# Kernel tuning notes

Measured on AMD Instinct MI355X. Metric: run time of the kernel, lower is better.

Reference implementation:

```python
import jax, jax.numpy as jnp
import numpy as np

HEADS = 16

def setup_inputs() -> dict:
    key = jax.random.key(0)
    k1, k2, k3, k4 = jax.random.split(key, 4)
    B, T, S, W = 2, 2048, 2048, 1024
    x = jax.random.normal(k1, (B, T, W), dtype=jnp.float32)
    cond_k = jax.random.normal(k2, (B, S, W), dtype=jnp.float32)
    cond_v = jax.random.normal(k3, (B, S, W), dtype=jnp.float32)
    w_proj = jax.random.normal(k4, (W, W), dtype=jnp.float32) * 0.02
    b_proj = jnp.zeros((W,), dtype=jnp.float32)
    return {"x": x, "cond_k": cond_k, "cond_v": cond_v, "w_proj": w_proj, "b_proj": b_proj}

def reference(x, cond_k, cond_v, w_proj, b_proj):
    B, T, W = x.shape
    S = cond_k.shape[1]
    H = HEADS
    d = W // H
    scale = 1.0 / jnp.sqrt(jnp.sqrt(jnp.float32(d)))  # applied to both q and k
    q = x.reshape(B, T, H, d) * scale
    k = cond_k.reshape(B, S, H, d) * scale
    v = cond_v.reshape(B, S, H, d)
    # scores: [B, H, T, S]
    scores = jnp.einsum('bthd,bshd->bhts', q, k)
    w = jax.nn.softmax(scores.astype(jnp.float32), axis=-1).astype(scores.dtype)
    out = jnp.einsum('bhts,bshd->bthd', w, v).reshape(B, T, W)
    # c_proj: torch Linear -> x @ W.T + b
    return out @ w_proj.T + b_proj
```

## Files before the change

kernel.cpp:

```cpp
#include <hip/hip_runtime.h>

#define Bn 2
#define Hn 16
#define Tn 2048
#define Sn 2048
#define Wd 1024
#define Dh 64

typedef __attribute__((ext_vector_type(8))) short s16x8;
typedef __attribute__((ext_vector_type(4))) short s16x4;
typedef __attribute__((ext_vector_type(4))) float f32x4;
typedef __attribute__((ext_vector_type(4))) unsigned u32x4;

#define MFMA(a, b, c) __builtin_amdgcn_mfma_f32_16x16x32_bf16((a), (b), (c), 0, 0, 0)

__device__ __forceinline__ s16x8 ld8(const short* p) { return *(const s16x8*)p; }

__device__ __forceinline__ short f2bf(float f) {
    unsigned u = __builtin_bit_cast(unsigned, f);
    u += 0x7FFFu + ((u >> 16) & 1u);
    return (short)(u >> 16);
}

__device__ __forceinline__ unsigned cvtpk(float lo, float hi) {
    unsigned r;
    asm("v_cvt_pk_bf16_f32 %0, %1, %2" : "=v"(r) : "v"(lo), "v"(hi));
    return r;
}

__device__ __forceinline__ void gl_lds(const short* g, short* lds) {
    __builtin_amdgcn_global_load_lds(
        (const __attribute__((address_space(1))) void*)g,
        (__attribute__((address_space(3))) void*)lds, 16, 0, 0);
}

__global__ __launch_bounds__(256) void prep(const float* __restrict__ ck,
                                            const float* __restrict__ cv,
                                            const float* __restrict__ wp,
                                            short* __restrict__ kp,
                                            short* __restrict__ vp,
                                            short* __restrict__ wb)
{
    __shared__ short T[64][72];
    const int blk = blockIdx.x;
    const int tid = threadIdx.x;
    if (blk < 2048) {
        const int isV = blk >> 10;
        const int c   = blk & 1023;
        const int bh = c >> 5, sc = c & 31;
        const int b = bh >> 4, h = bh & 15;
        const float* src = (isV ? cv : ck) + (size_t)(b * Sn + sc * 64) * Wd + h * Dh;
#pragma unroll
        for (int i = 0; i < 4; ++i) {
            int f = i * 256 + tid, sr = f >> 4, c4 = f & 15;
            float4 v = *(const float4*)(src + (size_t)sr * Wd + c4 * 4);
            s16x4 o;
            o[0] = f2bf(v.x); o[1] = f2bf(v.y); o[2] = f2bf(v.z); o[3] = f2bf(v.w);
            *(s16x4*)&T[sr][c4 * 4] = o;
        }
        __syncthreads();
        const int rt = tid >> 6;
        const int l = tid & 63, quad = l >> 4, l16 = l & 15;
        if (!isV) {
            size_t base = ((size_t)((bh * 128 + sc * 4 + rt) * 2)) * 512 + l * 8;
            *(s16x8*)(kp + base)       = *(const s16x8*)&T[rt * 16 + l16][quad * 8];
            *(s16x8*)(kp + base + 512) = *(const s16x8*)&T[rt * 16 + l16][32 + quad * 8];
        } else {
#pragma unroll
            for (int g = 0; g < 2; ++g) {
                s16x8 o;
#pragma unroll
                for (int j = 0; j < 8; ++j) {
                    int s = 32 * g + 16 * (j >> 2) + quad * 4 + (j & 3);
                    o[j] = T[s][rt * 16 + l16];
                }
                *(s16x8*)(vp + ((size_t)((bh * 32 + sc) * 8 + rt * 2 + g)) * 512 + l * 8) = o;
            }
        }
    } else {
        int i = ((blk - 2048) * 256 + tid) * 8;
        float4 a = *(const float4*)(wp + i);
        float4 b = *(const float4*)(wp + i + 4);
        s16x8 o;
        o[0] = f2bf(a.x); o[1] = f2bf(a.y); o[2] = f2bf(a.z); o[3] = f2bf(a.w);
        o[4] = f2bf(b.x); o[5] = f2bf(b.y); o[6] = f2bf(b.z); o[7] = f2bf(b.w);
        *(s16x8*)(wb + i) = o;
    }
}

__global__ __launch_bounds__(512, 4) void attn_fused(
    const float* __restrict__ x, const short* __restrict__ kp,
    const short* __restrict__ vt, short* __restrict__ ao)
{
    __shared__ alignas(16) short Ks[2][2][8 * 512];
    __shared__ alignas(16) short Vs[2][2][8 * 512];

    const int tid  = threadIdx.x;
    const int w    = tid >> 6;
    const int l    = tid & 63;
    const int quad = l >> 4;
    const int l16  = l & 15;
    const int wq   = w & 3;
    const int pr   = w >> 2;

    const int bh = blockIdx.x & 31;
    const int qt = blockIdx.x >> 5;
    const int b  = bh >> 4, h = bh & 15;

    const int qrow0 = qt * 128 + wq * 32;

    const short* kp_h = kp + (size_t)bh * 131072;
    const short* vp_h = vt + (size_t)bh * 131072;

    gl_lds(kp_h + ((size_t)(0 * 8 + w)) * 512 + l * 8, &Ks[0][0][w * 512]);
    gl_lds(vp_h + ((size_t)(0 * 8 + w)) * 512 + l * 8, &Vs[0][0][w * 512]);
    gl_lds(kp_h + ((size_t)(1 * 8 + w)) * 512 + l * 8, &Ks[0][1][w * 512]);
    gl_lds(vp_h + ((size_t)(1 * 8 + w)) * 512 + l * 8, &Vs[0][1][w * 512]);

    const float SQ = 0.125f * 1.4426950408889634f;
    s16x8 aq[2][2];
#pragma unroll
    for (int mi = 0; mi < 2; ++mi)
#pragma unroll
        for (int c = 0; c < 2; ++c) {
            const float* p = x + (size_t)(b * Tn + qrow0 + mi * 16 + l16) * Wd
                               + h * Dh + c * 32 + quad * 8;
            float4 a = ((const float4*)p)[0], bb = ((const float4*)p)[1];
            s16x8 o;
            o[0] = f2bf(a.x * SQ); o[1] = f2bf(a.y * SQ); o[2] = f2bf(a.z * SQ); o[3] = f2bf(a.w * SQ);
            o[4] = f2bf(bb.x * SQ); o[5] = f2bf(bb.y * SQ); o[6] = f2bf(bb.z * SQ); o[7] = f2bf(bb.w * SQ);
            aq[mi][c] = o;
        }

    f32x4 oacc[2][4], dnacc[2];
#pragma unroll
    for (int mi = 0; mi < 2; ++mi) {
#pragma unroll
        for (int nt = 0; nt < 4; ++nt) {
            oacc[mi][nt][0] = 0.f; oacc[mi][nt][1] = 0.f;
            oacc[mi][nt][2] = 0.f; oacc[mi][nt][3] = 0.f;
        }
        dnacc[mi][0] = 0.f; dnacc[mi][1] = 0.f;
        dnacc[mi][2] = 0.f; dnacc[mi][3] = 0.f;
    }

    s16x8 ones;
#pragma unroll
    for (int j = 0; j < 8; ++j) ones[j] = (short)0x3F80;

    const f32x4 z = {0.f, 0.f, 0.f, 0.f};
    const int NSIT = Sn / 128;

    asm volatile("s_waitcnt vmcnt(0)" ::: "memory");
    __syncthreads();

    for (int t = 0; t < NSIT; ++t) {
        const int sb = t & 1;

        if (t + 1 < NSIT) {
            const size_t c0 = (size_t)(2 * t + 2) * 8;
            gl_lds(kp_h + (c0 + w) * 512 + l * 8,     &Ks[sb ^ 1][0][w * 512]);
            gl_lds(vp_h + (c0 + w) * 512 + l * 8,     &Vs[sb ^ 1][0][w * 512]);
            gl_lds(kp_h + (c0 + 8 + w) * 512 + l * 8, &Ks[sb ^ 1][1][w * 512]);
            gl_lds(vp_h + (c0 + 8 + w) * 512 + l * 8, &Vs[sb ^ 1][1][w * 512]);
        }

        const short* Kb = &Ks[sb][pr][0];
        const short* Vb = &Vs[sb][pr][0];

        s16x8 kf[4][2];
#pragma unroll
        for (int sj = 0; sj < 4; ++sj)
#pragma unroll
            for (int g = 0; g < 2; ++g)
                kf[sj][g] = *(const s16x8*)&Kb[(sj * 2 + g) * 512 + l * 8];

        f32x4 sc[2][4];
        __builtin_amdgcn_s_setprio(1);
#pragma unroll
        for (int sj = 0; sj < 4; ++sj)
#pragma unroll
            for (int mi = 0; mi < 2; ++mi) {
                sc[mi][sj] = MFMA(kf[sj][0], aq[mi][0], z);
                sc[mi][sj] = MFMA(kf[sj][1], aq[mi][1], sc[mi][sj]);
            }
        __builtin_amdgcn_s_setprio(0);

        s16x8 ap[2][2];
#pragma unroll
        for (int mi = 0; mi < 2; ++mi) {
            float ex[4][4];
#pragma unroll
            for (int sj = 0; sj < 4; ++sj)
#pragma unroll
                for (int r = 0; r < 4; ++r)
                    ex[sj][r] = __builtin_amdgcn_exp2f(sc[mi][sj][r]);
#pragma unroll
            for (int g = 0; g < 2; ++g) {
                u32x4 pk;
                pk[0] = cvtpk(ex[2 * g][0],     ex[2 * g][1]);
                pk[1] = cvtpk(ex[2 * g][2],     ex[2 * g][3]);
                pk[2] = cvtpk(ex[2 * g + 1][0], ex[2 * g + 1][1]);
                pk[3] = cvtpk(ex[2 * g + 1][2], ex[2 * g + 1][3]);
                ap[mi][g] = __builtin_bit_cast(s16x8, pk);
            }
        }

        s16x8 vf[4][2];
#pragma unroll
        for (int nt = 0; nt < 4; ++nt)
#pragma unroll
            for (int g = 0; g < 2; ++g)
                vf[nt][g] = *(const s16x8*)&Vb[(nt * 2 + g) * 512 + l * 8];

        __builtin_amdgcn_s_setprio(1);
#pragma unroll
        for (int mi = 0; mi < 2; ++mi) {
            dnacc[mi] = MFMA(ap[mi][0], ones, dnacc[mi]);
            dnacc[mi] = MFMA(ap[mi][1], ones, dnacc[mi]);
        }
#pragma unroll
        for (int mi = 0; mi < 2; ++mi)
#pragma unroll
            for (int nt = 0; nt < 4; ++nt) {
                oacc[mi][nt] = MFMA(ap[mi][0], vf[nt][0], oacc[mi][nt]);
                oacc[mi][nt] = MFMA(ap[mi][1], vf[nt][1], oacc[mi][nt]);
            }
        __builtin_amdgcn_s_setprio(0);

        asm volatile("s_waitcnt vmcnt(0)" ::: "memory");
        __syncthreads();
    }

    float* ob = (float*)&Ks[0][0][0];
    float* db = (float*)&Vs[0][0][0];
    if (pr == 1) {
#pragma unroll
        for (int mi = 0; mi < 2; ++mi) {
#pragma unroll
            for (int r = 0; r < 4; ++r) {
                int ql = wq * 32 + mi * 16 + quad * 4 + r;
#pragma unroll
                for (int nt = 0; nt < 4; ++nt)
                    ob[ql * 64 + nt * 16 + l16] = oacc[mi][nt][r];
                if (l16 == 0) db[ql] = dnacc[mi][r];
            }
        }
    }
    __syncthreads();
    if (pr == 0) {
#pragma unroll
        for (int mi = 0; mi < 2; ++mi)
#pragma unroll
            for (int r = 0; r < 4; ++r) {
                int ql = wq * 32 + mi * 16 + quad * 4 + r;
                float inv = 1.0f / (dnacc[mi][r] + db[ql]);
                int t = qrow0 + mi * 16 + quad * 4 + r;
#pragma unroll
                for (int nt = 0; nt < 4; ++nt) {
                    float v = oacc[mi][nt][r] + ob[ql * 64 + nt * 16 + l16];
                    ao[(size_t)(b * Tn + t) * Wd + h * Dh + nt * 16 + l16] = f2bf(v * inv);
                }
            }
    }
}

#define LSTR2 72

__global__ __launch_bounds__(512, 4) void proj_gemm(
    const short* __restrict__ A, const short* __restrict__ Wb,
    const float* __restrict__ bias, float* __restrict__ out)
{
    __shared__ alignas(16) short As[2][128 * LSTR2];
    __shared__ alignas(16) short Bs[2][64 * LSTR2];

    const int tid  = threadIdx.x;
    const int w    = tid >> 6;
    const int l    = tid & 63;
    const int quad = l >> 4;
    const int l16  = l & 15;

    const int bn = blockIdx.x & 15;
    const int bm = blockIdx.x >> 4;
    const int m0 = bm * 128;
    const int n0 = bn * 64;
    const int wm = (w & 3) * 32;
    const int wn = (w >> 2) * 32;

    const int rr = tid >> 3;
    const int sg = tid & 7;

    f32x4 acc[2][2];
#pragma unroll
    for (int mi = 0; mi < 2; ++mi)
#pragma unroll
        for (int nt = 0; nt < 2; ++nt) {
            acc[mi][nt][0] = 0.f; acc[mi][nt][1] = 0.f;
            acc[mi][nt][2] = 0.f; acc[mi][nt][3] = 0.f;
        }

    s16x8 ra0 = ld8(A  + (size_t)(m0 + rr) * Wd + sg * 8);
    s16x8 ra1 = ld8(A  + (size_t)(m0 + 64 + rr) * Wd + sg * 8);
    s16x8 rb  = ld8(Wb + (size_t)(n0 + rr) * Wd + sg * 8);
    *(s16x8*)&As[0][rr * LSTR2 + sg * 8]        = ra0;
    *(s16x8*)&As[0][(rr + 64) * LSTR2 + sg * 8] = ra1;
    *(s16x8*)&Bs[0][rr * LSTR2 + sg * 8]        = rb;
    __syncthreads();

    for (int k0 = 0; k0 < Wd; k0 += 64) {
        const int p = (k0 >> 6) & 1;

        if (k0 + 64 < Wd) {
            ra0 = ld8(A  + (size_t)(m0 + rr) * Wd + k0 + 64 + sg * 8);
            ra1 = ld8(A  + (size_t)(m0 + 64 + rr) * Wd + k0 + 64 + sg * 8);
            rb  = ld8(Wb + (size_t)(n0 + rr) * Wd + k0 + 64 + sg * 8);
        }

        s16x8 a[2][2], bw[2][2];
#pragma unroll
        for (int mi = 0; mi < 2; ++mi)
#pragma unroll
            for (int ks = 0; ks < 2; ++ks)
                a[mi][ks] = *(const s16x8*)&As[p][(wm + mi * 16 + l16) * LSTR2 + ks * 32 + quad * 8];
#pragma unroll
        for (int nt = 0; nt < 2; ++nt)
#pragma unroll
            for (int ks = 0; ks < 2; ++ks)
                bw[nt][ks] = *(const s16x8*)&Bs[p][(wn + nt * 16 + l16) * LSTR2 + ks * 32 + quad * 8];

        __builtin_amdgcn_s_setprio(1);
#pragma unroll
        for (int mi = 0; mi < 2; ++mi)
#pragma unroll
            for (int nt = 0; nt < 2; ++nt) {
                acc[mi][nt] = MFMA(a[mi][0], bw[nt][0], acc[mi][nt]);
                acc[mi][nt] = MFMA(a[mi][1], bw[nt][1], acc[mi][nt]);
            }
        __builtin_amdgcn_s_setprio(0);

        if (k0 + 64 < Wd) {
            *(s16x8*)&As[p ^ 1][rr * LSTR2 + sg * 8]        = ra0;
            *(s16x8*)&As[p ^ 1][(rr + 64) * LSTR2 + sg * 8] = ra1;
            *(s16x8*)&Bs[p ^ 1][rr * LSTR2 + sg * 8]        = rb;
        }
        __syncthreads();
    }

#pragma unroll
    for (int nt = 0; nt < 2; ++nt) {
        float bv = bias[n0 + wn + nt * 16 + l16];
#pragma unroll
        for (int mi = 0; mi < 2; ++mi)
#pragma unroll
            for (int r = 0; r < 4; ++r)
                out[(size_t)(m0 + wm + mi * 16 + quad * 4 + r) * Wd + n0 + wn + nt * 16 + l16] =
                    acc[mi][nt][r] + bv;
    }
}

extern "C" void kernel_launch(void* const* d_in, const int* in_sizes, int n_in,
                              void* d_out, int out_size, void* d_ws, size_t ws_size,
                              hipStream_t stream) {
    const float* x  = (const float*)d_in[0];
    const float* ck = (const float*)d_in[1];
    const float* cv = (const float*)d_in[2];
    const float* wp = (const float*)d_in[3];
    const float* bp = (const float*)d_in[4];

    const int nX = Bn * Tn * Wd;
    const int nW = Wd * Wd;

    short* kpb = (short*)d_ws;
    short* vpb = kpb + nX;
    short* wbb = vpb + nX;
    short* am  = wbb + nW;

    prep<<<dim3(2048 + nW / 2048), dim3(256), 0, stream>>>(ck, cv, wp, kpb, vpb, wbb);

    attn_fused<<<dim3(Bn * Hn * (Tn / 128)), dim3(512), 0, stream>>>(x, kpb, vpb, am);
    proj_gemm<<<dim3((Bn * Tn / 128) * (Wd / 64)), dim3(512), 0, stream>>>(
        am, wbb, bp, (float*)d_out);
}
```

Measured before the change: 148.9 us.

## Pre-pack projection weights into MFMA fragments and stream A via global_load_lds

The prep kernel now converts w_proj into per-16-row MFMA fragment tiles, so proj_gemm can load B operands directly from global memory into registers with no LDS staging. The A operand is brought in with direct global-to-LDS loads into an XOR-swizzled unpadded layout instead of going through registers. This removes the B shared-memory buffer and the register round trip for A. The cost is a full vmcnt wait each iteration and B fragments read from global/L2 by every block that needs them.

```diff
diff --git a/kernel.cpp b/kernel.cpp
--- a/kernel.cpp
+++ b/kernel.cpp
@@ -41,7 +41,7 @@
                                             short* __restrict__ vp,
                                             short* __restrict__ wb)
 {
-    __shared__ short T[64][72];
+    __shared__ short T[64 * 72];
     const int blk = blockIdx.x;
     const int tid = threadIdx.x;
     if (blk < 2048) {
@@ -56,15 +56,15 @@
             float4 v = *(const float4*)(src + (size_t)sr * Wd + c4 * 4);
             s16x4 o;
             o[0] = f2bf(v.x); o[1] = f2bf(v.y); o[2] = f2bf(v.z); o[3] = f2bf(v.w);
-            *(s16x4*)&T[sr][c4 * 4] = o;
+            *(s16x4*)&T[sr * 72 + c4 * 4] = o;
         }
         __syncthreads();
         const int rt = tid >> 6;
         const int l = tid & 63, quad = l >> 4, l16 = l & 15;
         if (!isV) {
             size_t base = ((size_t)((bh * 128 + sc * 4 + rt) * 2)) * 512 + l * 8;
-            *(s16x8*)(kp + base)       = *(const s16x8*)&T[rt * 16 + l16][quad * 8];
-            *(s16x8*)(kp + base + 512) = *(const s16x8*)&T[rt * 16 + l16][32 + quad * 8];
+            *(s16x8*)(kp + base)       = *(const s16x8*)&T[(rt * 16 + l16) * 72 + quad * 8];
+            *(s16x8*)(kp + base + 512) = *(const s16x8*)&T[(rt * 16 + l16) * 72 + 32 + quad * 8];
         } else {
 #pragma unroll
             for (int g = 0; g < 2; ++g) {
@@ -72,19 +72,30 @@
 #pragma unroll
                 for (int j = 0; j < 8; ++j) {
                     int s = 32 * g + 16 * (j >> 2) + quad * 4 + (j & 3);
-                    o[j] = T[s][rt * 16 + l16];
+                    o[j] = T[s * 72 + rt * 16 + l16];
                 }
                 *(s16x8*)(vp + ((size_t)((bh * 32 + sc) * 8 + rt * 2 + g)) * 512 + l * 8) = o;
             }
         }
     } else {
-        int i = ((blk - 2048) * 256 + tid) * 8;
-        float4 a = *(const float4*)(wp + i);
-        float4 b = *(const float4*)(wp + i + 4);
-        s16x8 o;
-        o[0] = f2bf(a.x); o[1] = f2bf(a.y); o[2] = f2bf(a.z); o[3] = f2bf(a.w);
-        o[4] = f2bf(b.x); o[5] = f2bf(b.y); o[6] = f2bf(b.z); o[7] = f2bf(b.w);
-        *(s16x8*)(wb + i) = o;
+        const int c = blk - 2048;
+        const int tr = c >> 4, tc = c & 15;
+#pragma unroll
+        for (int i = 0; i < 4; ++i) {
+            int f = i * 256 + tid, sr = f >> 4, c4 = f & 15;
+            float4 v = *(const float4*)(wp + (size_t)(tr * 64 + sr) * Wd + tc * 64 + c4 * 4);
+            s16x4 o;
+            o[0] = f2bf(v.x); o[1] = f2bf(v.y); o[2] = f2bf(v.z); o[3] = f2bf(v.w);
+            *(s16x4*)&T[sr * 72 + c4 * 4] = o;
+        }
+        __syncthreads();
+        const int rt = tid >> 6;
+        const int l = tid & 63, quad = l >> 4, l16 = l & 15;
+#pragma unroll
+        for (int gl = 0; gl < 2; ++gl) {
+            size_t base = ((size_t)((tr * 4 + rt) * 32 + tc * 2 + gl)) * 512 + l * 8;
+            *(s16x8*)(wb + base) = *(const s16x8*)&T[(rt * 16 + l16) * 72 + gl * 32 + quad * 8];
+        }
     }
 }
 
@@ -265,14 +276,11 @@
     }
 }
 
-#define LSTR2 72
-
 __global__ __launch_bounds__(512, 4) void proj_gemm(
-    const short* __restrict__ A, const short* __restrict__ Wb,
+    const short* __restrict__ A, const short* __restrict__ wbp,
     const float* __restrict__ bias, float* __restrict__ out)
 {
-    __shared__ alignas(16) short As[2][128 * LSTR2];
-    __shared__ alignas(16) short Bs[2][64 * LSTR2];
+    __shared__ alignas(16) short As[2][128 * 64];
 
     const int tid  = threadIdx.x;
     const int w    = tid >> 6;
@@ -286,9 +294,10 @@
     const int n0 = bn * 64;
     const int wm = (w & 3) * 32;
     const int wn = (w >> 2) * 32;
-
-    const int rr = tid >> 3;
-    const int sg = tid & 7;
+    const int n16b = bn * 4 + (w >> 2) * 2;
+
+    const int rl0 = w * 16 + (l >> 3);
+    const int b16 = l & 7;
 
     f32x4 acc[2][2];
 #pragma unroll
@@ -299,34 +308,43 @@
             acc[mi][nt][2] = 0.f; acc[mi][nt][3] = 0.f;
         }
 
-    s16x8 ra0 = ld8(A  + (size_t)(m0 + rr) * Wd + sg * 8);
-    s16x8 ra1 = ld8(A  + (size_t)(m0 + 64 + rr) * Wd + sg * 8);
-    s16x8 rb  = ld8(Wb + (size_t)(n0 + rr) * Wd + sg * 8);
-    *(s16x8*)&As[0][rr * LSTR2 + sg * 8]        = ra0;
-    *(s16x8*)&As[0][(rr + 64) * LSTR2 + sg * 8] = ra1;
-    *(s16x8*)&Bs[0][rr * LSTR2 + sg * 8]        = rb;
+#pragma unroll
+    for (int u = 0; u < 2; ++u) {
+        int row = rl0 + u * 8;
+        gl_lds(A + (size_t)(m0 + row) * Wd + ((b16 ^ (row & 7)) * 8),
+               &As[0][(w * 16 + u * 8) * 64]);
+    }
+    asm volatile("s_waitcnt vmcnt(0)" ::: "memory");
     __syncthreads();
 
     for (int k0 = 0; k0 < Wd; k0 += 64) {
         const int p = (k0 >> 6) & 1;
+        const int kg = k0 >> 5;
+
+        s16x8 bw[2][2];
+#pragma unroll
+        for (int nt = 0; nt < 2; ++nt)
+#pragma unroll
+            for (int ks = 0; ks < 2; ++ks)
+                bw[nt][ks] = ld8(wbp + ((size_t)(n16b + nt) * 32 + kg + ks) * 512 + l * 8);
 
         if (k0 + 64 < Wd) {
-            ra0 = ld8(A  + (size_t)(m0 + rr) * Wd + k0 + 64 + sg * 8);
-            ra1 = ld8(A  + (size_t)(m0 + 64 + rr) * Wd + k0 + 64 + sg * 8);
-            rb  = ld8(Wb + (size_t)(n0 + rr) * Wd + k0 + 64 + sg * 8);
-        }
-
-        s16x8 a[2][2], bw[2][2];
-#pragma unroll
-        for (int mi = 0; mi < 2; ++mi)
+#pragma unroll
+            for (int u = 0; u < 2; ++u) {
+                int row = rl0 + u * 8;
+                gl_lds(A + (size_t)(m0 + row) * Wd + k0 + 64 + ((b16 ^ (row & 7)) * 8),
+                       &As[p ^ 1][(w * 16 + u * 8) * 64]);
+            }
+        }
+
+        s16x8 a[2][2];
+#pragma unroll
+        for (int mi = 0; mi < 2; ++mi) {
+            const int row = wm + mi * 16 + l16;
 #pragma unroll
             for (int ks = 0; ks < 2; ++ks)
-                a[mi][ks] = *(const s16x8*)&As[p][(wm + mi * 16 + l16) * LSTR2 + ks * 32 + quad * 8];
-#pragma unroll
-        for (int nt = 0; nt < 2; ++nt)
-#pragma unroll
-            for (int ks = 0; ks < 2; ++ks)
-                bw[nt][ks] = *(const s16x8*)&Bs[p][(wn + nt * 16 + l16) * LSTR2 + ks * 32 + quad * 8];
+                a[mi][ks] = *(const s16x8*)&As[p][row * 64 + ((ks * 4 + quad) ^ (row & 7)) * 8];
+        }
 
         __builtin_amdgcn_s_setprio(1);
 #pragma unroll
@@ -338,11 +356,7 @@
             }
         __builtin_amdgcn_s_setprio(0);
 
-        if (k0 + 64 < Wd) {
-            *(s16x8*)&As[p ^ 1][rr * LSTR2 + sg * 8]        = ra0;
-            *(s16x8*)&As[p ^ 1][(rr + 64) * LSTR2 + sg * 8] = ra1;
-            *(s16x8*)&Bs[p ^ 1][rr * LSTR2 + sg * 8]        = rb;
-        }
+        asm volatile("s_waitcnt vmcnt(0)" ::: "memory");
         __syncthreads();
     }
 
@@ -375,7 +389,7 @@
     short* wbb = vpb + nX;
     short* am  = wbb + nW;
 
-    prep<<<dim3(2048 + nW / 2048), dim3(256), 0, stream>>>(ck, cv, wp, kpb, vpb, wbb);
+    prep<<<dim3(2048 + 256), dim3(256), 0, stream>>>(ck, cv, wp, kpb, vpb, wbb);
 
     attn_fused<<<dim3(Bn * Hn * (Tn / 128)), dim3(512), 0, stream>>>(x, kpb, vpb, am);
     proj_gemm<<<dim3((Bn * Tn / 128) * (Wd / 64)), dim3(512), 0, stream>>>(
```

New measurement: 150.2 us. No clear change (+0.9%).

## Fuse prep, attention and projection into one persistent kernel with grid barriers

Applied to the files above, without the earlier changes.

Merges the three kernels into a single persistent kernel of 512 blocks that runs the bf16 conversion/relayout work in a strided task loop, crosses a software global barrier, runs attention, crosses another barrier, and then runs the output projection GEMM. The shared memory is unified into one buffer reused by each phase. This removes two kernel launch boundaries and their tail/drain gaps, but adds atomic spin barriers and requires all 512 blocks to be co-resident (occupancy 4 blocks per CU assumed), and the prep phase now uses only half the threads for the store step.

```diff
diff --git a/kernel.cpp b/kernel.cpp
--- a/kernel.cpp
+++ b/kernel.cpp
@@ -6,6 +6,7 @@
 #define Sn 2048
 #define Wd 1024
 #define Dh 64
+#define NBLK 512
 
 typedef __attribute__((ext_vector_type(8))) short s16x8;
 typedef __attribute__((ext_vector_type(4))) short s16x4;
@@ -34,327 +35,352 @@
         (__attribute__((address_space(3))) void*)lds, 16, 0, 0);
 }
 
-__global__ __launch_bounds__(256) void prep(const float* __restrict__ ck,
-                                            const float* __restrict__ cv,
-                                            const float* __restrict__ wp,
-                                            short* __restrict__ kp,
-                                            short* __restrict__ vp,
-                                            short* __restrict__ wb)
+__global__ void binit(unsigned* bar) { bar[0] = 0u; bar[1] = 0u; }
+
+__device__ __forceinline__ void gbar(unsigned* bar) {
+    __syncthreads();
+    if (threadIdx.x == 0) {
+        __builtin_amdgcn_fence(__ATOMIC_RELEASE, "agent");
+        unsigned g = __hip_atomic_load(&bar[1], __ATOMIC_ACQUIRE,
+                                       __HIP_MEMORY_SCOPE_AGENT);
+        unsigned arr = __hip_atomic_fetch_add(&bar[0], 1u, __ATOMIC_ACQ_REL,
+                                              __HIP_MEMORY_SCOPE_AGENT);
+        if (arr == NBLK - 1u) {
+            __hip_atomic_store(&bar[0], 0u, __ATOMIC_RELAXED,
+                               __HIP_MEMORY_SCOPE_AGENT);
+            __hip_atomic_fetch_add(&bar[1], 1u, __ATOMIC_RELEASE,
+                                   __HIP_MEMORY_SCOPE_AGENT);
+        } else {
+            long spins = 0;
+            while (__hip_atomic_load(&bar[1], __ATOMIC_ACQUIRE,
+                                     __HIP_MEMORY_SCOPE_AGENT) == g) {
+                __builtin_amdgcn_s_sleep(2);
+                if (++spins > (1L << 26)) break;
+            }
+        }
+    }
+    __syncthreads();
+    __builtin_amdgcn_fence(__ATOMIC_ACQUIRE, "agent");
+}
+
+__global__ __launch_bounds__(512, 4) void fused(
+    const float* __restrict__ x,  const float* __restrict__ ck,
+    const float* __restrict__ cv, const float* __restrict__ wp,
+    const float* __restrict__ bias,
+    short* __restrict__ kp, short* __restrict__ vp, short* __restrict__ wb,
+    short* __restrict__ am, float* __restrict__ out, unsigned* __restrict__ bar)
 {
-    __shared__ short T[64][72];
-    const int blk = blockIdx.x;
-    const int tid = threadIdx.x;
-    if (blk < 2048) {
-        const int isV = blk >> 10;
-        const int c   = blk & 1023;
-        const int bh = c >> 5, sc = c & 31;
-        const int b = bh >> 4, h = bh & 15;
-        const float* src = (isV ? cv : ck) + (size_t)(b * Sn + sc * 64) * Wd + h * Dh;
-#pragma unroll
-        for (int i = 0; i < 4; ++i) {
-            int f = i * 256 + tid, sr = f >> 4, c4 = f & 15;
-            float4 v = *(const float4*)(src + (size_t)sr * Wd + c4 * 4);
-            s16x4 o;
-            o[0] = f2bf(v.x); o[1] = f2bf(v.y); o[2] = f2bf(v.z); o[3] = f2bf(v.w);
-            *(s16x4*)&T[sr][c4 * 4] = o;
-        }
-        __syncthreads();
-        const int rt = tid >> 6;
-        const int l = tid & 63, quad = l >> 4, l16 = l & 15;
-        if (!isV) {
-            size_t base = ((size_t)((bh * 128 + sc * 4 + rt) * 2)) * 512 + l * 8;
-            *(s16x8*)(kp + base)       = *(const s16x8*)&T[rt * 16 + l16][quad * 8];
-            *(s16x8*)(kp + base + 512) = *(const s16x8*)&T[rt * 16 + l16][32 + quad * 8];
-        } else {
-#pragma unroll
-            for (int g = 0; g < 2; ++g) {
-                s16x8 o;
-#pragma unroll
-                for (int j = 0; j < 8; ++j) {
-                    int s = 32 * g + 16 * (j >> 2) + quad * 4 + (j & 3);
-                    o[j] = T[s][rt * 16 + l16];
-                }
-                *(s16x8*)(vp + ((size_t)((bh * 32 + sc) * 8 + rt * 2 + g)) * 512 + l * 8) = o;
-            }
-        }
-    } else {
-        int i = ((blk - 2048) * 256 + tid) * 8;
-        float4 a = *(const float4*)(wp + i);
-        float4 b = *(const float4*)(wp + i + 4);
-        s16x8 o;
-        o[0] = f2bf(a.x); o[1] = f2bf(a.y); o[2] = f2bf(a.z); o[3] = f2bf(a.w);
-        o[4] = f2bf(b.x); o[5] = f2bf(b.y); o[6] = f2bf(b.z); o[7] = f2bf(b.w);
-        *(s16x8*)(wb + i) = o;
-    }
-}
-
-__global__ __launch_bounds__(512, 4) void attn_fused(
-    const float* __restrict__ x, const short* __restrict__ kp,
-    const short* __restrict__ vt, short* __restrict__ ao)
-{
-    __shared__ alignas(16) short Ks[2][2][8 * 512];
-    __shared__ alignas(16) short Vs[2][2][8 * 512];
+    __shared__ alignas(16) short U[32768];
 
     const int tid  = threadIdx.x;
+    const int bid  = blockIdx.x;
     const int w    = tid >> 6;
     const int l    = tid & 63;
     const int quad = l >> 4;
     const int l16  = l & 15;
-    const int wq   = w & 3;
-    const int pr   = w >> 2;
-
-    const int bh = blockIdx.x & 31;
-    const int qt = blockIdx.x >> 5;
-    const int b  = bh >> 4, h = bh & 15;
-
-    const int qrow0 = qt * 128 + wq * 32;
-
-    const short* kp_h = kp + (size_t)bh * 131072;
-    const short* vp_h = vt + (size_t)bh * 131072;
-
-    gl_lds(kp_h + ((size_t)(0 * 8 + w)) * 512 + l * 8, &Ks[0][0][w * 512]);
-    gl_lds(vp_h + ((size_t)(0 * 8 + w)) * 512 + l * 8, &Vs[0][0][w * 512]);
-    gl_lds(kp_h + ((size_t)(1 * 8 + w)) * 512 + l * 8, &Ks[0][1][w * 512]);
-    gl_lds(vp_h + ((size_t)(1 * 8 + w)) * 512 + l * 8, &Vs[0][1][w * 512]);
-
-    const float SQ = 0.125f * 1.4426950408889634f;
-    s16x8 aq[2][2];
-#pragma unroll
-    for (int mi = 0; mi < 2; ++mi)
-#pragma unroll
-        for (int c = 0; c < 2; ++c) {
-            const float* p = x + (size_t)(b * Tn + qrow0 + mi * 16 + l16) * Wd
-                               + h * Dh + c * 32 + quad * 8;
-            float4 a = ((const float4*)p)[0], bb = ((const float4*)p)[1];
+
+    for (int task = bid; task < 2304; task += 512) {
+        __syncthreads();
+        if (task < 2048) {
+            const int isV = task >> 10;
+            const int c   = task & 1023;
+            const int bh = c >> 5, sc = c & 31;
+            const int b = bh >> 4, h = bh & 15;
+            const float* src = (isV ? cv : ck) + (size_t)(b * Sn + sc * 64) * Wd + h * Dh;
+#pragma unroll
+            for (int i = 0; i < 2; ++i) {
+                int f = i * 512 + tid, sr = f >> 4, c4 = f & 15;
+                float4 v = *(const float4*)(src + (size_t)sr * Wd + c4 * 4);
+                s16x4 o;
+                o[0] = f2bf(v.x); o[1] = f2bf(v.y); o[2] = f2bf(v.z); o[3] = f2bf(v.w);
+                *(s16x4*)&U[sr * 72 + c4 * 4] = o;
+            }
+            __syncthreads();
+            if (tid < 256) {
+                const int rt = tid >> 6;
+                if (!isV) {
+                    size_t base = ((size_t)((bh * 128 + sc * 4 + rt) * 2)) * 512 + l * 8;
+                    *(s16x8*)(kp + base)       = *(const s16x8*)&U[(rt * 16 + l16) * 72 + quad * 8];
+                    *(s16x8*)(kp + base + 512) = *(const s16x8*)&U[(rt * 16 + l16) * 72 + 32 + quad * 8];
+                } else {
+#pragma unroll
+                    for (int g = 0; g < 2; ++g) {
+                        s16x8 o;
+#pragma unroll
+                        for (int j = 0; j < 8; ++j) {
+                            int s = 32 * g + 16 * (j >> 2) + quad * 4 + (j & 3);
+                            o[j] = U[s * 72 + rt * 16 + l16];
+                        }
+                        *(s16x8*)(vp + ((size_t)((bh * 32 + sc) * 8 + rt * 2 + g)) * 512 + l * 8) = o;
+                    }
+                }
+            }
+        } else {
+            int i = ((task - 2048) * 512 + tid) * 8;
+            float4 a = *(const float4*)(wp + i);
+            float4 b2 = *(const float4*)(wp + i + 4);
             s16x8 o;
-            o[0] = f2bf(a.x * SQ); o[1] = f2bf(a.y * SQ); o[2] = f2bf(a.z * SQ); o[3] = f2bf(a.w * SQ);
-            o[4] = f2bf(bb.x * SQ); o[5] = f2bf(bb.y * SQ); o[6] = f2bf(bb.z * SQ); o[7] = f2bf(bb.w * SQ);
-            aq[mi][c] = o;
-        }
-
-    f32x4 oacc[2][4], dnacc[2];
-#pragma unroll
-    for (int mi = 0; mi < 2; ++mi) {
-#pragma unroll
-        for (int nt = 0; nt < 4; ++nt) {
-            oacc[mi][nt][0] = 0.f; oacc[mi][nt][1] = 0.f;
-            oacc[mi][nt][2] = 0.f; oacc[mi][nt][3] = 0.f;
-        }
-        dnacc[mi][0] = 0.f; dnacc[mi][1] = 0.f;
-        dnacc[mi][2] = 0.f; dnacc[mi][3] = 0.f;
+            o[0] = f2bf(a.x); o[1] = f2bf(a.y); o[2] = f2bf(a.z); o[3] = f2bf(a.w);
+            o[4] = f2bf(b2.x); o[5] = f2bf(b2.y); o[6] = f2bf(b2.z); o[7] = f2bf(b2.w);
+            *(s16x8*)(wb + i) = o;
+        }
     }
-
-    s16x8 ones;
-#pragma unroll
-    for (int j = 0; j < 8; ++j) ones[j] = (short)0x3F80;
-
-    const f32x4 z = {0.f, 0.f, 0.f, 0.f};
-    const int NSIT = Sn / 128;
-
-    asm volatile("s_waitcnt vmcnt(0)" ::: "memory");
-    __syncthreads();
-
-    for (int t = 0; t < NSIT; ++t) {
-        const int sb = t & 1;
-
-        if (t + 1 < NSIT) {
-            const size_t c0 = (size_t)(2 * t + 2) * 8;
-            gl_lds(kp_h + (c0 + w) * 512 + l * 8,     &Ks[sb ^ 1][0][w * 512]);
-            gl_lds(vp_h + (c0 + w) * 512 + l * 8,     &Vs[sb ^ 1][0][w * 512]);
-            gl_lds(kp_h + (c0 + 8 + w) * 512 + l * 8, &Ks[sb ^ 1][1][w * 512]);
-            gl_lds(vp_h + (c0 + 8 + w) * 512 + l * 8, &Vs[sb ^ 1][1][w * 512]);
-        }
-
-        const short* Kb = &Ks[sb][pr][0];
-        const short* Vb = &Vs[sb][pr][0];
-
-        s16x8 kf[4][2];
-#pragma unroll
-        for (int sj = 0; sj < 4; ++sj)
-#pragma unroll
-            for (int g = 0; g < 2; ++g)
-                kf[sj][g] = *(const s16x8*)&Kb[(sj * 2 + g) * 512 + l * 8];
-
-        f32x4 sc[2][4];
-        __builtin_amdgcn_s_setprio(1);
-#pragma unroll
-        for (int sj = 0; sj < 4; ++sj)
-#pragma unroll
-            for (int mi = 0; mi < 2; ++mi) {
-                sc[mi][sj] = MFMA(kf[sj][0], aq[mi][0], z);
-                sc[mi][sj] = MFMA(kf[sj][1], aq[mi][1], sc[mi][sj]);
-            }
-        __builtin_amdgcn_s_setprio(0);
-
-        s16x8 ap[2][2];
+    gbar(bar);
+
+    {
+        short* const KsB = U;
+        short* const VsB = U + 16384;
+
+        const int wq = w & 3;
+        const int pr = w >> 2;
+
+        const int bh = bid & 31;
+        const int qt = bid >> 5;
+        const int b  = bh >> 4, h = bh & 15;
+
+        const int qrow0 = qt * 128 + wq * 32;
+
+        const short* kp_h = kp + (size_t)bh * 131072;
+        const short* vp_h = vp + (size_t)bh * 131072;
+
+        gl_lds(kp_h + ((size_t)(0 * 8 + w)) * 512 + l * 8, KsB + 0 * 4096 + w * 512);
+        gl_lds(vp_h + ((size_t)(0 * 8 + w)) * 512 + l * 8, VsB + 0 * 4096 + w * 512);
+        gl_lds(kp_h + ((size_t)(1 * 8 + w)) * 512 + l * 8, KsB + 1 * 4096 + w * 512);
+        gl_lds(vp_h + ((size_t)(1 * 8 + w)) * 512 + l * 8, VsB + 1 * 4096 + w * 512);
+
+        const float SQ = 0.125f * 1.4426950408889634f;
+        s16x8 aq[2][2];
+#pragma unroll
+        for (int mi = 0; mi < 2; ++mi)
+#pragma unroll
+            for (int c = 0; c < 2; ++c) {
+                const float* p = x + (size_t)(b * Tn + qrow0 + mi * 16 + l16) * Wd
+                                   + h * Dh + c * 32 + quad * 8;
+                float4 a = ((const float4*)p)[0], bb = ((const float4*)p)[1];
+                s16x8 o;
+                o[0] = f2bf(a.x * SQ); o[1] = f2bf(a.y * SQ); o[2] = f2bf(a.z * SQ); o[3] = f2bf(a.w * SQ);
+                o[4] = f2bf(bb.x * SQ); o[5] = f2bf(bb.y * SQ); o[6] = f2bf(bb.z * SQ); o[7] = f2bf(bb.w * SQ);
+                aq[mi][c] = o;
+            }
+
+        f32x4 oacc[2][4], dnacc[2];
 #pragma unroll
         for (int mi = 0; mi < 2; ++mi) {
-            float ex[4][4];
-#pragma unroll
-            for (int sj = 0; sj < 4; ++sj)
-#pragma unroll
-                for (int r = 0; r < 4; ++r)
-                    ex[sj][r] = __builtin_amdgcn_exp2f(sc[mi][sj][r]);
-#pragma unroll
-            for (int g = 0; g < 2; ++g) {
-                u32x4 pk;
-                pk[0] = cvtpk(ex[2 * g][0],     ex[2 * g][1]);
-                pk[1] = cvtpk(ex[2 * g][2],     ex[2 * g][3]);
-                pk[2] = cvtpk(ex[2 * g + 1][0], ex[2 * g + 1][1]);
-                pk[3] = cvtpk(ex[2 * g + 1][2], ex[2 * g + 1][3]);
-                ap[mi][g] = __builtin_bit_cast(s16x8, pk);
-            }
-        }
-
-        s16x8 vf[4][2];
-#pragma unroll
-        for (int nt = 0; nt < 4; ++nt)
-#pragma unroll
-            for (int g = 0; g < 2; ++g)
-                vf[nt][g] = *(const s16x8*)&Vb[(nt * 2 + g) * 512 + l * 8];
-
-        __builtin_amdgcn_s_setprio(1);
-#pragma unroll
-        for (int mi = 0; mi < 2; ++mi) {
-            dnacc[mi] = MFMA(ap[mi][0], ones, dnacc[mi]);
-            dnacc[mi] = MFMA(ap[mi][1], ones, dnacc[mi]);
-        }
-#pragma unroll
-        for (int mi = 0; mi < 2; ++mi)
 #pragma unroll
             for (int nt = 0; nt < 4; ++nt) {
-                oacc[mi][nt] = MFMA(ap[mi][0], vf[nt][0], oacc[mi][nt]);
-                oacc[mi][nt] = MFMA(ap[mi][1], vf[nt][1], oacc[mi][nt]);
-            }
-        __builtin_amdgcn_s_setprio(0);
+                oacc[mi][nt][0] = 0.f; oacc[mi][nt][1] = 0.f;
+                oacc[mi][nt][2] = 0.f; oacc[mi][nt][3] = 0.f;
+            }
+            dnacc[mi][0] = 0.f; dnacc[mi][1] = 0.f;
+            dnacc[mi][2] = 0.f; dnacc[mi][3] = 0.f;
+        }
+
+        s16x8 ones;
+#pragma unroll
+        for (int j = 0; j < 8; ++j) ones[j] = (short)0x3F80;
+
+        const f32x4 z = {0.f, 0.f, 0.f, 0.f};
+        const int NSIT = Sn / 128;
 
         asm volatile("s_waitcnt vmcnt(0)" ::: "memory");
         __syncthreads();
+
+        for (int t = 0; t < NSIT; ++t) {
+            const int sb = t & 1;
+
+            if (t + 1 < NSIT) {
+                const size_t c0 = (size_t)(2 * t + 2) * 8;
+                gl_lds(kp_h + (c0 + w) * 512 + l * 8,     KsB + ((sb ^ 1) * 2 + 0) * 4096 + w * 512);
+                gl_lds(vp_h + (c0 + w) * 512 + l * 8,     VsB + ((sb ^ 1) * 2 + 0) * 4096 + w * 512);
+                gl_lds(kp_h + (c0 + 8 + w) * 512 + l * 8, KsB + ((sb ^ 1) * 2 + 1) * 4096 + w * 512);
+                gl_lds(vp_h + (c0 + 8 + w) * 512 + l * 8, VsB + ((sb ^ 1) * 2 + 1) * 4096 + w * 512);
+            }
+
+            const short* Kb = KsB + (sb * 2 + pr) * 4096;
+            const short* Vb = VsB + (sb * 2 + pr) * 4096;
+
+            s16x8 kf[4][2];
+#pragma unroll
+            for (int sj = 0; sj < 4; ++sj)
+#pragma unroll
+                for (int g = 0; g < 2; ++g)
+                    kf[sj][g] = *(const s16x8*)&Kb[(sj * 2 + g) * 512 + l * 8];
+
+            f32x4 sc[2][4];
+            __builtin_amdgcn_s_setprio(1);
+#pragma unroll
+            for (int sj = 0; sj < 4; ++sj)
+#pragma unroll
+                for (int mi = 0; mi < 2; ++mi) {
+                    sc[mi][sj] = MFMA(kf[sj][0], aq[mi][0], z);
+                    sc[mi][sj] = MFMA(kf[sj][1], aq[mi][1], sc[mi][sj]);
+                }
+            __builtin_amdgcn_s_setprio(0);
+
+            s16x8 ap[2][2];
+#pragma unroll
+            for (int mi = 0; mi < 2; ++mi) {
+                float ex[4][4];
+#pragma unroll
+                for (int sj = 0; sj < 4; ++sj)
+#pragma unroll
+                    for (int r = 0; r < 4; ++r)
+                        ex[sj][r] = __builtin_amdgcn_exp2f(sc[mi][sj][r]);
+#pragma unroll
+                for (int g = 0; g < 2; ++g) {
+                    u32x4 pk;
+                    pk[0] = cvtpk(ex[2 * g][0],     ex[2 * g][1]);
+                    pk[1] = cvtpk(ex[2 * g][2],     ex[2 * g][3]);
+                    pk[2] = cvtpk(ex[2 * g + 1][0], ex[2 * g + 1][1]);
+                    pk[3] = cvtpk(ex[2 * g + 1][2], ex[2 * g + 1][3]);
+                    ap[mi][g] = __builtin_bit_cast(s16x8, pk);
+                }
+            }
+
+            s16x8 vf[4][2];
+#pragma unroll
+            for (int nt = 0; nt < 4; ++nt)
+#pragma unroll
+                for (int g = 0; g < 2; ++g)
+                    vf[nt][g] = *(const s16x8*)&Vb[(nt * 2 + g) * 512 + l * 8];
+
+            __builtin_amdgcn_s_setprio(1);
+#pragma unroll
+            for (int mi = 0; mi < 2; ++mi) {
+                dnacc[mi] = MFMA(ap[mi][0], ones, dnacc[mi]);
+                dnacc[mi] = MFMA(ap[mi][1], ones, dnacc[mi]);
+            }
+#pragma unroll
+            for (int mi = 0; mi < 2; ++mi)
+#pragma unroll
+                for (int nt = 0; nt < 4; ++nt) {
+                    oacc[mi][nt] = MFMA(ap[mi][0], vf[nt][0], oacc[mi][nt]);
+                    oacc[mi][nt] = MFMA(ap[mi][1], vf[nt][1], oacc[mi][nt]);
+                }
+            __builtin_amdgcn_s_setprio(0);
+
+            asm volatile("s_waitcnt vmcnt(0)" ::: "memory");
+            __syncthreads();
+        }
+
+        float* ob = (float*)U;
+        float* db = (float*)(U + 16384);
+        if (pr == 1) {
+#pragma unroll
+            for (int mi = 0; mi < 2; ++mi) {
+#pragma unroll
+                for (int r = 0; r < 4; ++r) {
+                    int ql = wq * 32 + mi * 16 + quad * 4 + r;
+#pragma unroll
+                    for (int nt = 0; nt < 4; ++nt)
+                        ob[ql * 64 + nt * 16 + l16] = oacc[mi][nt][r];
+                    if (l16 == 0) db[ql] = dnacc[mi][r];
+                }
+            }
+        }
+        __syncthreads();
+        if (pr == 0) {
+#pragma unroll
+            for (int mi = 0; mi < 2; ++mi)
+#pragma unroll
+                for (int r = 0; r < 4; ++r) {
+                    int ql = wq * 32 + mi * 16 + quad * 4 + r;
+                    float inv = 1.0f / (dnacc[mi][r] + db[ql]);
+                    int t = qrow0 + mi * 16 + quad * 4 + r;
+#pragma unroll
+                    for (int nt = 0; nt < 4; ++nt) {
+                        float v = oacc[mi][nt][r] + ob[ql * 64 + nt * 16 + l16];
+                        am[(size_t)(b * Tn + t) * Wd + h * Dh + nt * 16 + l16] = f2bf(v * inv);
+                    }
+                }
+        }
     }
-
-    float* ob = (float*)&Ks[0][0][0];
-    float* db = (float*)&Vs[0][0][0];
-    if (pr == 1) {
-#pragma unroll
-        for (int mi = 0; mi < 2; ++mi) {
-#pragma unroll
-            for (int r = 0; r < 4; ++r) {
-                int ql = wq * 32 + mi * 16 + quad * 4 + r;
-#pragma unroll
-                for (int nt = 0; nt < 4; ++nt)
-                    ob[ql * 64 + nt * 16 + l16] = oacc[mi][nt][r];
-                if (l16 == 0) db[ql] = dnacc[mi][r];
-            }
-        }
-    }
-    __syncthreads();
-    if (pr == 0) {
+    gbar(bar);
+
+    {
+        short* const AsB = U;
+        short* const BsB = U + 18432;
+
+        const int bn = bid & 15;
+        const int bm = bid >> 4;
+        const int m0 = bm * 128;
+        const int n0 = bn * 64;
+        const int wm = (w & 3) * 32;
+        const int wn = (w >> 2) * 32;
+
+        const int rr = tid >> 3;
+        const int sg = tid & 7;
+
+        f32x4 acc[2][2];
 #pragma unroll
         for (int mi = 0; mi < 2; ++mi)
 #pragma unroll
-            for (int r = 0; r < 4; ++r) {
-                int ql = wq * 32 + mi * 16 + quad * 4 + r;
-                float inv = 1.0f / (dnacc[mi][r] + db[ql]);
-                int t = qrow0 + mi * 16 + quad * 4 + r;
-#pragma unroll
-                for (int nt = 0; nt < 4; ++nt) {
-                    float v = oacc[mi][nt][r] + ob[ql * 64 + nt * 16 + l16];
-                    ao[(size_t)(b * Tn + t) * Wd + h * Dh + nt * 16 + l16] = f2bf(v * inv);
-                }
-            }
-    }
-}
-
-#define LSTR2 72
-
-__global__ __launch_bounds__(512, 4) void proj_gemm(
-    const short* __restrict__ A, const short* __restrict__ Wb,
-    const float* __restrict__ bias, float* __restrict__ out)
-{
-    __shared__ alignas(16) short As[2][128 * LSTR2];
-    __shared__ alignas(16) short Bs[2][64 * LSTR2];
-
-    const int tid  = threadIdx.x;
-    const int w    = tid >> 6;
-    const int l    = tid & 63;
-    const int quad = l >> 4;
-    const int l16  = l & 15;
-
-    const int bn = blockIdx.x & 15;
-    const int bm = blockIdx.x >> 4;
-    const int m0 = bm * 128;
-    const int n0 = bn * 64;
-    const int wm = (w & 3) * 32;
-    const int wn = (w >> 2) * 32;
-
-    const int rr = tid >> 3;
-    const int sg = tid & 7;
-
-    f32x4 acc[2][2];
-#pragma unroll
-    for (int mi = 0; mi < 2; ++mi)
+            for (int nt = 0; nt < 2; ++nt) {
+                acc[mi][nt][0] = 0.f; acc[mi][nt][1] = 0.f;
+                acc[mi][nt][2] = 0.f; acc[mi][nt][3] = 0.f;
+            }
+
+        s16x8 ra0 = ld8(am + (size_t)(m0 + rr) * Wd + sg * 8);
+        s16x8 ra1 = ld8(am + (size_t)(m0 + 64 + rr) * Wd + sg * 8);
+        s16x8 rb  = ld8(wb + (size_t)(n0 + rr) * Wd + sg * 8);
+        *(s16x8*)&AsB[rr * 72 + sg * 8]        = ra0;
+        *(s16x8*)&AsB[(rr + 64) * 72 + sg * 8] = ra1;
+        *(s16x8*)&BsB[rr * 72 + sg * 8]        = rb;
+        __syncthreads();
+
+        for (int k0 = 0; k0 < Wd; k0 += 64) {
+            const int p = (k0 >> 6) & 1;
+            short* Asp = AsB + p * 9216;
+            short* Bsp = BsB + p * 4608;
+
+            if (k0 + 64 < Wd) {
+                ra0 = ld8(am + (size_t)(m0 + rr) * Wd + k0 + 64 + sg * 8);
+                ra1 = ld8(am + (size_t)(m0 + 64 + rr) * Wd + k0 + 64 + sg * 8);
+                rb  = ld8(wb + (size_t)(n0 + rr) * Wd + k0 + 64 + sg * 8);
+            }
+
+            s16x8 a[2][2], bw[2][2];
+#pragma unroll
+            for (int mi = 0; mi < 2; ++mi)
+#pragma unroll
+                for (int ks = 0; ks < 2; ++ks)
+                    a[mi][ks] = *(const s16x8*)&Asp[(wm + mi * 16 + l16) * 72 + ks * 32 + quad * 8];
+#pragma unroll
+            for (int nt = 0; nt < 2; ++nt)
+#pragma unroll
+                for (int ks = 0; ks < 2; ++ks)
+                    bw[nt][ks] = *(const s16x8*)&Bsp[(wn + nt * 16 + l16) * 72 + ks * 32 + quad * 8];
+
+            __builtin_amdgcn_s_setprio(1);
+#pragma unroll
+            for (int mi = 0; mi < 2; ++mi)
+#pragma unroll
+                for (int nt = 0; nt < 2; ++nt) {
+                    acc[mi][nt] = MFMA(a[mi][0], bw[nt][0], acc[mi][nt]);
+                    acc[mi][nt] = MFMA(a[mi][1], bw[nt][1], acc[mi][nt]);
+                }
+            __builtin_amdgcn_s_setprio(0);
+
+            if (k0 + 64 < Wd) {
+                short* Asn = AsB + (p ^ 1) * 9216;
+                short* Bsn = BsB + (p ^ 1) * 4608;
+                *(s16x8*)&Asn[rr * 72 + sg * 8]        = ra0;
+                *(s16x8*)&Asn[(rr + 64) * 72 + sg * 8] = ra1;
+                *(s16x8*)&Bsn[rr * 72 + sg * 8]        = rb;
+            }
+            __syncthreads();
+        }
+
 #pragma unroll
         for (int nt = 0; nt < 2; ++nt) {
-            acc[mi][nt][0] = 0.f; acc[mi][nt][1] = 0.f;
-            acc[mi][nt][2] = 0.f; acc[mi][nt][3] = 0.f;
-        }
-
-    s16x8 ra0 = ld8(A  + (size_t)(m0 + rr) * Wd + sg * 8);
-    s16x8 ra1 = ld8(A  + (size_t)(m0 + 64 + rr) * Wd + sg * 8);
-    s16x8 rb  = ld8(Wb + (size_t)(n0 + rr) * Wd + sg * 8);
-    *(s16x8*)&As[0][rr * LSTR2 + sg * 8]        = ra0;
-    *(s16x8*)&As[0][(rr + 64) * LSTR2 + sg * 8] = ra1;
-    *(s16x8*)&Bs[0][rr * LSTR2 + sg * 8]        = rb;
-    __syncthreads();
-
-    for (int k0 = 0; k0 < Wd; k0 += 64) {
-        const int p = (k0 >> 6) & 1;
-
-        if (k0 + 64 < Wd) {
-            ra0 = ld8(A  + (size_t)(m0 + rr) * Wd + k0 + 64 + sg * 8);
-            ra1 = ld8(A  + (size_t)(m0 + 64 + rr) * Wd + k0 + 64 + sg * 8);
-            rb  = ld8(Wb + (size_t)(n0 + rr) * Wd + k0 + 64 + sg * 8);
-        }
-
-        s16x8 a[2][2], bw[2][2];
-#pragma unroll
-        for (int mi = 0; mi < 2; ++mi)
-#pragma unroll
-            for (int ks = 0; ks < 2; ++ks)
-                a[mi][ks] = *(const s16x8*)&As[p][(wm + mi * 16 + l16) * LSTR2 + ks * 32 + quad * 8];
-#pragma unroll
-        for (int nt = 0; nt < 2; ++nt)
-#pragma unroll
-            for (int ks = 0; ks < 2; ++ks)
-                bw[nt][ks] = *(const s16x8*)&Bs[p][(wn + nt * 16 + l16) * LSTR2 + ks * 32 + quad * 8];
-
-        __builtin_amdgcn_s_setprio(1);
-#pragma unroll
-        for (int mi = 0; mi < 2; ++mi)
-#pragma unroll
-            for (int nt = 0; nt < 2; ++nt) {
-                acc[mi][nt] = MFMA(a[mi][0], bw[nt][0], acc[mi][nt]);
-                acc[mi][nt] = MFMA(a[mi][1], bw[nt][1], acc[mi][nt]);
-            }
-        __builtin_amdgcn_s_setprio(0);
-
-        if (k0 + 64 < Wd) {
-            *(s16x8*)&As[p ^ 1][rr * LSTR2 + sg * 8]        = ra0;
-            *(s16x8*)&As[p ^ 1][(rr + 64) * LSTR2 + sg * 8] = ra1;
-            *(s16x8*)&Bs[p ^ 1][rr * LSTR2 + sg * 8]        = rb;
-        }
-        __syncthreads();
-    }
-
-#pragma unroll
-    for (int nt = 0; nt < 2; ++nt) {
-        float bv = bias[n0 + wn + nt * 16 + l16];
-#pragma unroll
-        for (int mi = 0; mi < 2; ++mi)
-#pragma unroll
-            for (int r = 0; r < 4; ++r)
-                out[(size_t)(m0 + wm + mi * 16 + quad * 4 + r) * Wd + n0 + wn + nt * 16 + l16] =
-                    acc[mi][nt][r] + bv;
+            float bv = bias[n0 + wn + nt * 16 + l16];
+#pragma unroll
+            for (int mi = 0; mi < 2; ++mi)
+#pragma unroll
+                for (int r = 0; r < 4; ++r)
+                    out[(size_t)(m0 + wm + mi * 16 + quad * 4 + r) * Wd + n0 + wn + nt * 16 + l16] =
+                        acc[mi][nt][r] + bv;
+        }
     }
 }
 
@@ -373,11 +399,11 @@
     short* kpb = (short*)d_ws;
     short* vpb = kpb + nX;
     short* wbb = vpb + nX;
-    short* am  = wbb + nW;
-
-    prep<<<dim3(2048 + nW / 2048), dim3(256), 0, stream>>>(ck, cv, wp, kpb, vpb, wbb);
-
-    attn_fused<<<dim3(Bn * Hn * (Tn / 128)), dim3(512), 0, stream>>>(x, kpb, vpb, am);
-    proj_gemm<<<dim3((Bn * Tn / 128) * (Wd / 64)), dim3(512), 0, stream>>>(
-        am, wbb, bp, (float*)d_out);
-}
+    short* amb = wbb + nW;
+    unsigned* bar = (unsigned*)(amb + nX);
+    float* op  = (float*)d_out;
+
+    binit<<<dim3(1), dim3(1), 0, stream>>>(bar);
+    fused<<<dim3(NBLK), dim3(512), 0, stream>>>(
+        x, ck, cv, wp, bp, kpb, vpb, wbb, amb, op, bar);
+}
```

New measurement: 387.7 us. 2.6x slower.
